# Optimization experiments

Hardware: AMD Instinct MI355X
Metric: run time of the kernel (lower is better)

## Reference

```python
import jax, jax.numpy as jnp
import numpy as np

N_NODES = 50000
N_EDGES = 800000
FEAT = 128
HID1 = 128
HID2 = 64


def setup_inputs() -> dict:
    key = jax.random.key(0)
    k = jax.random.split(key, 6)
    x = jax.random.normal(k[0], (N_NODES, FEAT), dtype=jnp.float32)
    edge_index = jax.random.randint(k[1], (2, N_EDGES), 0, N_NODES, dtype=jnp.int32)
    # Glorot-style init scaling like PyG's GCNConv linear
    W1 = jax.random.normal(k[2], (FEAT, HID1), dtype=jnp.float32) * (1.0 / np.sqrt(FEAT))
    b1 = jnp.zeros((HID1,), dtype=jnp.float32)
    W2 = jax.random.normal(k[3], (HID1, HID2), dtype=jnp.float32) * (1.0 / np.sqrt(HID1))
    b2 = jnp.zeros((HID2,), dtype=jnp.float32)
    return {"x": x, "edge_index": edge_index, "W1": W1, "b1": b1, "W2": W2, "b2": b2}


def _gcn_conv(x, src, dst, W, b, n_nodes):
    """PyG GCNConv: h = X W; out_i = sum_j norm_ij h_j + b, with self-loops and
    symmetric normalization norm_ij = deg_i^-1/2 * deg_j^-1/2 (deg counts self-loop)."""
    h = x @ W  # [N, out]
    # degree at target nodes (self-loops already appended to src/dst)
    deg = jax.ops.segment_sum(jnp.ones_like(dst, dtype=h.dtype), dst, num_segments=n_nodes)
    dinv = jax.lax.rsqrt(jnp.maximum(deg, 1.0))  # deg >= 1 because of self-loops
    norm = dinv[src] * dinv[dst]  # [E+N]
    msg = h[src] * norm[:, None]  # gather + scale, [E+N, out]
    out = jax.ops.segment_sum(msg, dst, num_segments=n_nodes)
    return out + b


def reference(x, edge_index, W1, b1, W2, b2):
    n = x.shape[0]
    self_idx = jnp.arange(n, dtype=edge_index.dtype)
    src = jnp.concatenate([edge_index[0], self_idx])
    dst = jnp.concatenate([edge_index[1], self_idx])
    h = jax.nn.relu(_gcn_conv(x, src, dst, W1, b1, n))
    out = _gcn_conv(h, src, dst, W2, b2, n)
    return out
```

## Files before the change

### kernel.cpp

```cpp
#include <hip/hip_runtime.h>
#include <hip/hip_bf16.h>


typedef __attribute__((ext_vector_type(8))) short short8;
typedef __attribute__((ext_vector_type(4))) float f32x4;

__device__ __forceinline__ float bf_lo(unsigned u) { return __uint_as_float(u << 16); }
__device__ __forceinline__ float bf_hi(unsigned u) { return __uint_as_float(u & 0xffff0000u); }
__device__ __forceinline__ unsigned short f2bf(float f) {
    return (unsigned short)(__bfloat16_as_ushort(__float2bfloat16(f)));
}

__global__ __launch_bounds__(256) void setup_kernel(int* __restrict__ cnt, int N,
                                                    const float* __restrict__ W1,
                                                    unsigned short* __restrict__ Wp1,
                                                    const float* __restrict__ W2,
                                                    unsigned short* __restrict__ Wp2) {
    int i = blockIdx.x * 256 + threadIdx.x;
    if (i < N + 1) {
        cnt[i] = 0;
    } else if (i < N + 1 + 128 * 128) {
        int q = i - (N + 1);
        int j = q & 7;
        int n = (q >> 3) & 127;
        int kb = q >> 10;
        Wp1[q] = f2bf(W1[(kb * 8 + j) * 128 + n]);
    } else if (i < N + 1 + 128 * 128 + 128 * 64) {
        int q = i - (N + 1) - 128 * 128;
        int j = q & 7;
        int n = (q >> 3) & 63;
        int kb = q >> 9;
        Wp2[q] = f2bf(W2[(kb * 8 + j) * 64 + n]);
    }
}

__global__ __launch_bounds__(256) void count_kernel(const int* __restrict__ dst,
                                                    int* __restrict__ cnt,
                                                    int* __restrict__ eslot, int E) {
    int e = blockIdx.x * 256 + threadIdx.x;
    if (e < E) eslot[e] = atomicAdd(&cnt[dst[e]], 1);
}

__global__ __launch_bounds__(256) void alloc_kernel(int* __restrict__ cnt,
                                                    int* __restrict__ row_ptr,
                                                    float* __restrict__ dinv, int N) {
    int i = blockIdx.x * 256 + threadIdx.x;
    int lane = threadIdx.x & 63;
    int c = (i < N) ? cnt[i] : 0;
    if (i < N) dinv[i] = rsqrtf((float)(c + 1));
    int incl = c;
#pragma unroll
    for (int off = 1; off < 64; off <<= 1) {
        int u = __shfl_up(incl, off, 64);
        if (lane >= off) incl += u;
    }
    int base = 0;
    if (lane == 63) base = atomicAdd(&cnt[N], incl);
    base = __shfl(base, 63, 64);
    if (i < N) row_ptr[i] = base + incl - c;
}

__global__ __launch_bounds__(256) void scatgemm_kernel(
    const int* __restrict__ src, const int* __restrict__ dst,
    const int* __restrict__ row_ptr, const int* __restrict__ eslot,
    int* __restrict__ ssrc, int E,
    const float* __restrict__ X, const unsigned short* __restrict__ Wp1,
    const float* __restrict__ dinv, unsigned short* __restrict__ g1,
    int N, int gb) {
    if ((int)blockIdx.x >= gb) {
        int e = (blockIdx.x - gb) * 256 + threadIdx.x;
        if (e < E) {
            int p = row_ptr[dst[e]] + eslot[e];
            ssrc[p] = src[e];
        }
        return;
    }
    constexpr int NT = 8;
    const int lane = threadIdx.x & 63;
    const int wave = threadIdx.x >> 6;
    const int col = lane & 15;
    const int quad = lane >> 4;
    const int row0w = (blockIdx.x * 4 + wave) * 16;

    int arow = row0w + col;
    if (arow >= N) arow = N - 1;

    short8 afr[4];
    const float* Xr = X + (size_t)arow * 128;
#pragma unroll
    for (int c = 0; c < 4; ++c) {
        float4 f0 = *(const float4*)(Xr + c * 32 + quad * 8);
        float4 f1 = *(const float4*)(Xr + c * 32 + quad * 8 + 4);
        short8 a;
        a[0] = (short)f2bf(f0.x); a[1] = (short)f2bf(f0.y);
        a[2] = (short)f2bf(f0.z); a[3] = (short)f2bf(f0.w);
        a[4] = (short)f2bf(f1.x); a[5] = (short)f2bf(f1.y);
        a[6] = (short)f2bf(f1.z); a[7] = (short)f2bf(f1.w);
        afr[c] = a;
    }

    f32x4 acc[NT];
#pragma unroll
    for (int t = 0; t < NT; ++t) acc[t] = (f32x4){0.f, 0.f, 0.f, 0.f};

    const uint4* Wq = (const uint4*)Wp1;
#pragma unroll
    for (int c = 0; c < 4; ++c) {
        short8 bfr[NT];
#pragma unroll
        for (int t = 0; t < NT; ++t) {
            union { uint4 u; short8 s; } cv;
            cv.u = Wq[(size_t)(c * 4 + quad) * 128 + t * 16 + col];
            bfr[t] = cv.s;
        }
#pragma unroll
        for (int t = 0; t < NT; ++t)
            acc[t] = __builtin_amdgcn_mfma_f32_16x16x32_bf16(afr[c], bfr[t], acc[t], 0, 0, 0);
    }

#pragma unroll
    for (int r = 0; r < 4; ++r) {
        int row = row0w + quad * 4 + r;
        if (row < N) {
            float dv = dinv[row];
#pragma unroll
            for (int t = 0; t < NT; ++t)
                g1[(size_t)row * 128 + t * 16 + col] = f2bf(acc[t][r] * dv);
        }
    }
}

template <int M>
__global__ __launch_bounds__(256) void mfma_gemm_kernel(const unsigned short* __restrict__ A,
                                                        const unsigned short* __restrict__ Wp,
                                                        const float* __restrict__ dinv,
                                                        unsigned short* __restrict__ C,
                                                        int N) {
    constexpr int NT = M / 16;
    const int lane = threadIdx.x & 63;
    const int wave = threadIdx.x >> 6;
    const int col = lane & 15;
    const int quad = lane >> 4;
    const int row0w = (blockIdx.x * 4 + wave) * 16;

    int arow = row0w + col;
    if (arow >= N) arow = N - 1;

    short8 afr[4];
    const uint4* Z = (const uint4*)A;
#pragma unroll
    for (int c = 0; c < 4; ++c) {
        union { uint4 u; short8 s; } cv;
        cv.u = Z[(size_t)arow * 16 + c * 4 + quad];
        afr[c] = cv.s;
    }

    f32x4 acc[NT];
#pragma unroll
    for (int t = 0; t < NT; ++t) acc[t] = (f32x4){0.f, 0.f, 0.f, 0.f};

    const uint4* Wq = (const uint4*)Wp;
#pragma unroll
    for (int c = 0; c < 4; ++c) {
        short8 bfr[NT];
#pragma unroll
        for (int t = 0; t < NT; ++t) {
            union { uint4 u; short8 s; } cv;
            cv.u = Wq[(size_t)(c * 4 + quad) * M + t * 16 + col];
            bfr[t] = cv.s;
        }
#pragma unroll
        for (int t = 0; t < NT; ++t)
            acc[t] = __builtin_amdgcn_mfma_f32_16x16x32_bf16(afr[c], bfr[t], acc[t], 0, 0, 0);
    }

#pragma unroll
    for (int r = 0; r < 4; ++r) {
        int row = row0w + quad * 4 + r;
        if (row < N) {
            float dv = dinv[row];
#pragma unroll
            for (int t = 0; t < NT; ++t)
                C[(size_t)row * M + t * 16 + col] = f2bf(acc[t][r] * dv);
        }
    }
}

template <int M, bool RELU, bool OUTBF16>
__global__ __launch_bounds__(256) void agg_kernel(const unsigned short* __restrict__ g,
                                                  const int* __restrict__ row_ptr,
                                                  const int* __restrict__ cnt,
                                                  const int* __restrict__ ssrc,
                                                  const float* __restrict__ dinv,
                                                  const float* __restrict__ bias,
                                                  void* __restrict__ outraw, int N) {
    int node = __builtin_amdgcn_readfirstlane((int)(blockIdx.x * 4 + (threadIdx.x >> 6)));
    if (node >= N) return;
    int lane = threadIdx.x & 63;
    float di = dinv[node];
    int beg = row_ptr[node];
    int end = beg + cnt[node];

    if constexpr (M == 128) {
        const unsigned* hp = (const unsigned*)g;
        unsigned hv = hp[node * 64 + lane];
        float ax0 = bf_lo(hv), ay0 = bf_hi(hv);
        float ax1 = 0.f, ay1 = 0.f;
        int j = beg;
        for (; j + 7 < end; j += 8) {
            int s0 = ssrc[j + 0], s1 = ssrc[j + 1], s2 = ssrc[j + 2], s3 = ssrc[j + 3];
            int s4 = ssrc[j + 4], s5 = ssrc[j + 5], s6 = ssrc[j + 6], s7 = ssrc[j + 7];
            unsigned v0 = hp[s0 * 64 + lane], v1 = hp[s1 * 64 + lane];
            unsigned v2 = hp[s2 * 64 + lane], v3 = hp[s3 * 64 + lane];
            unsigned v4 = hp[s4 * 64 + lane], v5 = hp[s5 * 64 + lane];
            unsigned v6 = hp[s6 * 64 + lane], v7 = hp[s7 * 64 + lane];
            ax0 += bf_lo(v0) + bf_lo(v1) + bf_lo(v2) + bf_lo(v3);
            ax1 += bf_lo(v4) + bf_lo(v5) + bf_lo(v6) + bf_lo(v7);
            ay0 += bf_hi(v0) + bf_hi(v1) + bf_hi(v2) + bf_hi(v3);
            ay1 += bf_hi(v4) + bf_hi(v5) + bf_hi(v6) + bf_hi(v7);
        }
        for (; j + 3 < end; j += 4) {
            int s0 = ssrc[j + 0], s1 = ssrc[j + 1], s2 = ssrc[j + 2], s3 = ssrc[j + 3];
            unsigned v0 = hp[s0 * 64 + lane], v1 = hp[s1 * 64 + lane];
            unsigned v2 = hp[s2 * 64 + lane], v3 = hp[s3 * 64 + lane];
            ax0 += bf_lo(v0) + bf_lo(v1);
            ax1 += bf_lo(v2) + bf_lo(v3);
            ay0 += bf_hi(v0) + bf_hi(v1);
            ay1 += bf_hi(v2) + bf_hi(v3);
        }
        for (; j < end; ++j) {
            unsigned v = hp[ssrc[j] * 64 + lane];
            ax0 += bf_lo(v);
            ay0 += bf_hi(v);
        }
        float ax = (ax0 + ax1) * di + bias[2 * lane];
        float ay = (ay0 + ay1) * di + bias[2 * lane + 1];
        if (RELU) { ax = fmaxf(ax, 0.f); ay = fmaxf(ay, 0.f); }
        if constexpr (OUTBF16) {
            unsigned pk = (unsigned)f2bf(ax) | ((unsigned)f2bf(ay) << 16);
            ((unsigned*)outraw)[node * 64 + lane] = pk;
        } else {
            ((float2*)outraw)[node * 64 + lane] = make_float2(ax, ay);
        }
    } else {
        float a0 = __uint_as_float((unsigned)g[node * 64 + lane] << 16);
        float a1 = 0.f;
        int j = beg;
        for (; j + 7 < end; j += 8) {
            int s0 = ssrc[j + 0], s1 = ssrc[j + 1], s2 = ssrc[j + 2], s3 = ssrc[j + 3];
            int s4 = ssrc[j + 4], s5 = ssrc[j + 5], s6 = ssrc[j + 6], s7 = ssrc[j + 7];
            float v0 = __uint_as_float((unsigned)g[s0 * 64 + lane] << 16);
            float v1 = __uint_as_float((unsigned)g[s1 * 64 + lane] << 16);
            float v2 = __uint_as_float((unsigned)g[s2 * 64 + lane] << 16);
            float v3 = __uint_as_float((unsigned)g[s3 * 64 + lane] << 16);
            float v4 = __uint_as_float((unsigned)g[s4 * 64 + lane] << 16);
            float v5 = __uint_as_float((unsigned)g[s5 * 64 + lane] << 16);
            float v6 = __uint_as_float((unsigned)g[s6 * 64 + lane] << 16);
            float v7 = __uint_as_float((unsigned)g[s7 * 64 + lane] << 16);
            a0 += v0 + v1 + v2 + v3;
            a1 += v4 + v5 + v6 + v7;
        }
        for (; j + 3 < end; j += 4) {
            int s0 = ssrc[j + 0], s1 = ssrc[j + 1], s2 = ssrc[j + 2], s3 = ssrc[j + 3];
            float v0 = __uint_as_float((unsigned)g[s0 * 64 + lane] << 16);
            float v1 = __uint_as_float((unsigned)g[s1 * 64 + lane] << 16);
            float v2 = __uint_as_float((unsigned)g[s2 * 64 + lane] << 16);
            float v3 = __uint_as_float((unsigned)g[s3 * 64 + lane] << 16);
            a0 += v0 + v1;
            a1 += v2 + v3;
        }
        for (; j < end; ++j)
            a0 += __uint_as_float((unsigned)g[ssrc[j] * 64 + lane] << 16);
        float acc = (a0 + a1) * di + bias[lane];
        if (RELU) acc = fmaxf(acc, 0.f);
        if constexpr (OUTBF16) {
            ((unsigned short*)outraw)[node * 64 + lane] = f2bf(acc);
        } else {
            ((float*)outraw)[node * 64 + lane] = acc;
        }
    }
}

extern "C" void kernel_launch(void* const* d_in, const int* in_sizes, int n_in,
                              void* d_out, int out_size, void* d_ws, size_t ws_size,
                              hipStream_t stream) {
    const float* x = (const float*)d_in[0];
    const int* eidx = (const int*)d_in[1];
    const float* W1 = (const float*)d_in[2];
    const float* b1 = (const float*)d_in[3];
    const float* W2 = (const float*)d_in[4];
    const float* b2 = (const float*)d_in[5];
    float* out = (float*)d_out;

    const int N = in_sizes[0] / 128;
    const int E = in_sizes[1] / 2;
    const int* src = eidx;
    const int* dst = eidx + E;

    char* ws = (char*)d_ws;
    size_t off = 0;
    auto alloc = [&](size_t bytes) -> char* {
        char* p = ws + off;
        off = (off + bytes + 255) & ~(size_t)255;
        return p;
    };
    int* cnt = (int*)alloc((size_t)(N + 1) * 4);
    int* row_ptr = (int*)alloc((size_t)N * 4);
    int* eslot = (int*)alloc((size_t)E * 4);
    int* ssrc = (int*)alloc((size_t)E * 4);
    float* dinv = (float*)alloc((size_t)N * 4);
    unsigned short* Wp1 = (unsigned short*)alloc(128 * 128 * 2);
    unsigned short* Wp2 = (unsigned short*)alloc(128 * 64 * 2);
    unsigned short* g1 = (unsigned short*)alloc((size_t)N * 128 * 2);
    unsigned short* z1 = (unsigned short*)alloc((size_t)N * 128 * 2);
    unsigned short* g2 = (unsigned short*)alloc((size_t)N * 64 * 2);

    const int nbN = (N + 255) / 256;
    const int nbE = (E + 255) / 256;
    const int gb = (N + 63) / 64;
    const int setup_n = N + 1 + 128 * 128 + 128 * 64;

    setup_kernel<<<(setup_n + 255) / 256, 256, 0, stream>>>(cnt, N, W1, Wp1, W2, Wp2);
    count_kernel<<<nbE, 256, 0, stream>>>(dst, cnt, eslot, E);
    alloc_kernel<<<nbN, 256, 0, stream>>>(cnt, row_ptr, dinv, N);
    scatgemm_kernel<<<gb + nbE, 256, 0, stream>>>(src, dst, row_ptr, eslot, ssrc, E,
                                                  x, Wp1, dinv, g1, N, gb);
    agg_kernel<128, true, true><<<(N + 3) / 4, 256, 0, stream>>>(g1, row_ptr, cnt, ssrc, dinv, b1, z1, N);
    mfma_gemm_kernel<64><<<gb, 256, 0, stream>>>(z1, Wp2, dinv, g2, N);
    agg_kernel<64, false, false><<<(N + 3) / 4, 256, 0, stream>>>(g2, row_ptr, cnt, ssrc, dinv, b2, out, N);
}
```

Baseline: 208.1 us.

## Fuse layer-1 aggregation with layer-2 GEMM via shared-memory tile

Merges the first-layer aggregation (with bias and ReLU) and the second-layer MFMA GEMM into one kernel. Each block aggregates 16 nodes into a bf16 tile in LDS, then each wave computes 16 output columns from that tile. This removes the z1 intermediate buffer and its global write and read, plus one kernel launch. In exchange, the gather phase now runs with 16 nodes per block and needs a __syncthreads before the GEMM, which could change latency hiding for the irregular gathers.

```diff
diff --git a/kernel.cpp b/kernel.cpp
--- a/kernel.cpp
+++ b/kernel.cpp
@@ -130,70 +130,106 @@
     }
 }
 
-template <int M>
-__global__ __launch_bounds__(256) void mfma_gemm_kernel(const unsigned short* __restrict__ A,
-                                                        const unsigned short* __restrict__ Wp,
-                                                        const float* __restrict__ dinv,
-                                                        unsigned short* __restrict__ C,
-                                                        int N) {
-    constexpr int NT = M / 16;
+__global__ __launch_bounds__(256) void aggmm_kernel(const unsigned short* __restrict__ g1,
+                                                    const int* __restrict__ row_ptr,
+                                                    const int* __restrict__ cnt,
+                                                    const int* __restrict__ ssrc,
+                                                    const float* __restrict__ dinv,
+                                                    const float* __restrict__ b1,
+                                                    const unsigned short* __restrict__ Wp2,
+                                                    unsigned short* __restrict__ g2, int N) {
+    __shared__ unsigned short zt[16][136];
+    __shared__ float sdinv[16];
     const int lane = threadIdx.x & 63;
     const int wave = threadIdx.x >> 6;
+    const int nodebase = blockIdx.x * 16;
+    const unsigned* hp = (const unsigned*)g1;
+
+    const float bx = b1[2 * lane];
+    const float by = b1[2 * lane + 1];
+
+#pragma unroll
+    for (int k = 0; k < 4; ++k) {
+        int zr = wave * 4 + k;
+        int node = __builtin_amdgcn_readfirstlane(nodebase + zr);
+        unsigned pk = 0;
+        if (node < N) {
+            float di = dinv[node];
+            int beg = row_ptr[node];
+            int end = beg + cnt[node];
+            unsigned hv = hp[node * 64 + lane];
+            float ax0 = bf_lo(hv), ay0 = bf_hi(hv);
+            float ax1 = 0.f, ay1 = 0.f;
+            int j = beg;
+            for (; j + 7 < end; j += 8) {
+                int s0 = ssrc[j + 0], s1 = ssrc[j + 1], s2 = ssrc[j + 2], s3 = ssrc[j + 3];
+                int s4 = ssrc[j + 4], s5 = ssrc[j + 5], s6 = ssrc[j + 6], s7 = ssrc[j + 7];
+                unsigned v0 = hp[s0 * 64 + lane], v1 = hp[s1 * 64 + lane];
+                unsigned v2 = hp[s2 * 64 + lane], v3 = hp[s3 * 64 + lane];
+                unsigned v4 = hp[s4 * 64 + lane], v5 = hp[s5 * 64 + lane];
+                unsigned v6 = hp[s6 * 64 + lane], v7 = hp[s7 * 64 + lane];
+                ax0 += bf_lo(v0) + bf_lo(v1) + bf_lo(v2) + bf_lo(v3);
+                ax1 += bf_lo(v4) + bf_lo(v5) + bf_lo(v6) + bf_lo(v7);
+                ay0 += bf_hi(v0) + bf_hi(v1) + bf_hi(v2) + bf_hi(v3);
+                ay1 += bf_hi(v4) + bf_hi(v5) + bf_hi(v6) + bf_hi(v7);
+            }
+            for (; j + 3 < end; j += 4) {
+                int s0 = ssrc[j + 0], s1 = ssrc[j + 1], s2 = ssrc[j + 2], s3 = ssrc[j + 3];
+                unsigned v0 = hp[s0 * 64 + lane], v1 = hp[s1 * 64 + lane];
+                unsigned v2 = hp[s2 * 64 + lane], v3 = hp[s3 * 64 + lane];
+                ax0 += bf_lo(v0) + bf_lo(v1);
+                ax1 += bf_lo(v2) + bf_lo(v3);
+                ay0 += bf_hi(v0) + bf_hi(v1);
+                ay1 += bf_hi(v2) + bf_hi(v3);
+            }
+            for (; j < end; ++j) {
+                unsigned v = hp[ssrc[j] * 64 + lane];
+                ax0 += bf_lo(v);
+                ay0 += bf_hi(v);
+            }
+            float ax = fmaxf((ax0 + ax1) * di + bx, 0.f);
+            float ay = fmaxf((ay0 + ay1) * di + by, 0.f);
+            pk = (unsigned)f2bf(ax) | ((unsigned)f2bf(ay) << 16);
+            if (lane == 0) sdinv[zr] = di;
+        } else if (lane == 0) {
+            sdinv[zr] = 0.f;
+        }
+        ((unsigned*)&zt[zr][0])[lane] = pk;
+    }
+    __syncthreads();
+
     const int col = lane & 15;
     const int quad = lane >> 4;
-    const int row0w = (blockIdx.x * 4 + wave) * 16;
-
-    int arow = row0w + col;
-    if (arow >= N) arow = N - 1;
-
     short8 afr[4];
-    const uint4* Z = (const uint4*)A;
 #pragma unroll
     for (int c = 0; c < 4; ++c) {
         union { uint4 u; short8 s; } cv;
-        cv.u = Z[(size_t)arow * 16 + c * 4 + quad];
+        cv.u = *(const uint4*)&zt[col][c * 32 + quad * 8];
         afr[c] = cv.s;
     }
-
-    f32x4 acc[NT];
-#pragma unroll
-    for (int t = 0; t < NT; ++t) acc[t] = (f32x4){0.f, 0.f, 0.f, 0.f};
-
-    const uint4* Wq = (const uint4*)Wp;
+    f32x4 acc = (f32x4){0.f, 0.f, 0.f, 0.f};
+    const uint4* Wq = (const uint4*)Wp2;
 #pragma unroll
     for (int c = 0; c < 4; ++c) {
-        short8 bfr[NT];
-#pragma unroll
-        for (int t = 0; t < NT; ++t) {
-            union { uint4 u; short8 s; } cv;
-            cv.u = Wq[(size_t)(c * 4 + quad) * M + t * 16 + col];
-            bfr[t] = cv.s;
-        }
-#pragma unroll
-        for (int t = 0; t < NT; ++t)
-            acc[t] = __builtin_amdgcn_mfma_f32_16x16x32_bf16(afr[c], bfr[t], acc[t], 0, 0, 0);
-    }
-
+        union { uint4 u; short8 s; } cv;
+        cv.u = Wq[(size_t)(c * 4 + quad) * 64 + wave * 16 + col];
+        acc = __builtin_amdgcn_mfma_f32_16x16x32_bf16(afr[c], cv.s, acc, 0, 0, 0);
+    }
 #pragma unroll
     for (int r = 0; r < 4; ++r) {
-        int row = row0w + quad * 4 + r;
-        if (row < N) {
-            float dv = dinv[row];
-#pragma unroll
-            for (int t = 0; t < NT; ++t)
-                C[(size_t)row * M + t * 16 + col] = f2bf(acc[t][r] * dv);
-        }
-    }
-}
-
-template <int M, bool RELU, bool OUTBF16>
-__global__ __launch_bounds__(256) void agg_kernel(const unsigned short* __restrict__ g,
-                                                  const int* __restrict__ row_ptr,
-                                                  const int* __restrict__ cnt,
-                                                  const int* __restrict__ ssrc,
-                                                  const float* __restrict__ dinv,
-                                                  const float* __restrict__ bias,
-                                                  void* __restrict__ outraw, int N) {
+        int row = nodebase + quad * 4 + r;
+        if (row < N)
+            g2[(size_t)row * 64 + wave * 16 + col] = f2bf(acc[r] * sdinv[quad * 4 + r]);
+    }
+}
+
+__global__ __launch_bounds__(256) void agg2_kernel(const unsigned short* __restrict__ g,
+                                                   const int* __restrict__ row_ptr,
+                                                   const int* __restrict__ cnt,
+                                                   const int* __restrict__ ssrc,
+                                                   const float* __restrict__ dinv,
+                                                   const float* __restrict__ bias,
+                                                   float* __restrict__ out, int N) {
     int node = __builtin_amdgcn_readfirstlane((int)(blockIdx.x * 4 + (threadIdx.x >> 6)));
     if (node >= N) return;
     int lane = threadIdx.x & 63;
@@ -201,84 +237,35 @@
     int beg = row_ptr[node];
     int end = beg + cnt[node];
 
-    if constexpr (M == 128) {
-        const unsigned* hp = (const unsigned*)g;
-        unsigned hv = hp[node * 64 + lane];
-        float ax0 = bf_lo(hv), ay0 = bf_hi(hv);
-        float ax1 = 0.f, ay1 = 0.f;
-        int j = beg;
-        for (; j + 7 < end; j += 8) {
-            int s0 = ssrc[j + 0], s1 = ssrc[j + 1], s2 = ssrc[j + 2], s3 = ssrc[j + 3];
-            int s4 = ssrc[j + 4], s5 = ssrc[j + 5], s6 = ssrc[j + 6], s7 = ssrc[j + 7];
-            unsigned v0 = hp[s0 * 64 + lane], v1 = hp[s1 * 64 + lane];
-            unsigned v2 = hp[s2 * 64 + lane], v3 = hp[s3 * 64 + lane];
-            unsigned v4 = hp[s4 * 64 + lane], v5 = hp[s5 * 64 + lane];
-            unsigned v6 = hp[s6 * 64 + lane], v7 = hp[s7 * 64 + lane];
-            ax0 += bf_lo(v0) + bf_lo(v1) + bf_lo(v2) + bf_lo(v3);
-            ax1 += bf_lo(v4) + bf_lo(v5) + bf_lo(v6) + bf_lo(v7);
-            ay0 += bf_hi(v0) + bf_hi(v1) + bf_hi(v2) + bf_hi(v3);
-            ay1 += bf_hi(v4) + bf_hi(v5) + bf_hi(v6) + bf_hi(v7);
-        }
-        for (; j + 3 < end; j += 4) {
-            int s0 = ssrc[j + 0], s1 = ssrc[j + 1], s2 = ssrc[j + 2], s3 = ssrc[j + 3];
-            unsigned v0 = hp[s0 * 64 + lane], v1 = hp[s1 * 64 + lane];
-            unsigned v2 = hp[s2 * 64 + lane], v3 = hp[s3 * 64 + lane];
-            ax0 += bf_lo(v0) + bf_lo(v1);
-            ax1 += bf_lo(v2) + bf_lo(v3);
-            ay0 += bf_hi(v0) + bf_hi(v1);
-            ay1 += bf_hi(v2) + bf_hi(v3);
-        }
-        for (; j < end; ++j) {
-            unsigned v = hp[ssrc[j] * 64 + lane];
-            ax0 += bf_lo(v);
-            ay0 += bf_hi(v);
-        }
-        float ax = (ax0 + ax1) * di + bias[2 * lane];
-        float ay = (ay0 + ay1) * di + bias[2 * lane + 1];
-        if (RELU) { ax = fmaxf(ax, 0.f); ay = fmaxf(ay, 0.f); }
-        if constexpr (OUTBF16) {
-            unsigned pk = (unsigned)f2bf(ax) | ((unsigned)f2bf(ay) << 16);
-            ((unsigned*)outraw)[node * 64 + lane] = pk;
-        } else {
-            ((float2*)outraw)[node * 64 + lane] = make_float2(ax, ay);
-        }
-    } else {
-        float a0 = __uint_as_float((unsigned)g[node * 64 + lane] << 16);
-        float a1 = 0.f;
-        int j = beg;
-        for (; j + 7 < end; j += 8) {
-            int s0 = ssrc[j + 0], s1 = ssrc[j + 1], s2 = ssrc[j + 2], s3 = ssrc[j + 3];
-            int s4 = ssrc[j + 4], s5 = ssrc[j + 5], s6 = ssrc[j + 6], s7 = ssrc[j + 7];
-            float v0 = __uint_as_float((unsigned)g[s0 * 64 + lane] << 16);
-            float v1 = __uint_as_float((unsigned)g[s1 * 64 + lane] << 16);
-            float v2 = __uint_as_float((unsigned)g[s2 * 64 + lane] << 16);
-            float v3 = __uint_as_float((unsigned)g[s3 * 64 + lane] << 16);
-            float v4 = __uint_as_float((unsigned)g[s4 * 64 + lane] << 16);
-            float v5 = __uint_as_float((unsigned)g[s5 * 64 + lane] << 16);
-            float v6 = __uint_as_float((unsigned)g[s6 * 64 + lane] << 16);
-            float v7 = __uint_as_float((unsigned)g[s7 * 64 + lane] << 16);
-            a0 += v0 + v1 + v2 + v3;
-            a1 += v4 + v5 + v6 + v7;
-        }
-        for (; j + 3 < end; j += 4) {
-            int s0 = ssrc[j + 0], s1 = ssrc[j + 1], s2 = ssrc[j + 2], s3 = ssrc[j + 3];
-            float v0 = __uint_as_float((unsigned)g[s0 * 64 + lane] << 16);
-            float v1 = __uint_as_float((unsigned)g[s1 * 64 + lane] << 16);
-            float v2 = __uint_as_float((unsigned)g[s2 * 64 + lane] << 16);
-            float v3 = __uint_as_float((unsigned)g[s3 * 64 + lane] << 16);
-            a0 += v0 + v1;
-            a1 += v2 + v3;
-        }
-        for (; j < end; ++j)
-            a0 += __uint_as_float((unsigned)g[ssrc[j] * 64 + lane] << 16);
-        float acc = (a0 + a1) * di + bias[lane];
-        if (RELU) acc = fmaxf(acc, 0.f);
-        if constexpr (OUTBF16) {
-            ((unsigned short*)outraw)[node * 64 + lane] = f2bf(acc);
-        } else {
-            ((float*)outraw)[node * 64 + lane] = acc;
-        }
-    }
+    float a0 = __uint_as_float((unsigned)g[node * 64 + lane] << 16);
+    float a1 = 0.f;
+    int j = beg;
+    for (; j + 7 < end; j += 8) {
+        int s0 = ssrc[j + 0], s1 = ssrc[j + 1], s2 = ssrc[j + 2], s3 = ssrc[j + 3];
+        int s4 = ssrc[j + 4], s5 = ssrc[j + 5], s6 = ssrc[j + 6], s7 = ssrc[j + 7];
+        float v0 = __uint_as_float((unsigned)g[s0 * 64 + lane] << 16);
+        float v1 = __uint_as_float((unsigned)g[s1 * 64 + lane] << 16);
+        float v2 = __uint_as_float((unsigned)g[s2 * 64 + lane] << 16);
+        float v3 = __uint_as_float((unsigned)g[s3 * 64 + lane] << 16);
+        float v4 = __uint_as_float((unsigned)g[s4 * 64 + lane] << 16);
+        float v5 = __uint_as_float((unsigned)g[s5 * 64 + lane] << 16);
+        float v6 = __uint_as_float((unsigned)g[s6 * 64 + lane] << 16);
+        float v7 = __uint_as_float((unsigned)g[s7 * 64 + lane] << 16);
+        a0 += v0 + v1 + v2 + v3;
+        a1 += v4 + v5 + v6 + v7;
+    }
+    for (; j + 3 < end; j += 4) {
+        int s0 = ssrc[j + 0], s1 = ssrc[j + 1], s2 = ssrc[j + 2], s3 = ssrc[j + 3];
+        float v0 = __uint_as_float((unsigned)g[s0 * 64 + lane] << 16);
+        float v1 = __uint_as_float((unsigned)g[s1 * 64 + lane] << 16);
+        float v2 = __uint_as_float((unsigned)g[s2 * 64 + lane] << 16);
+        float v3 = __uint_as_float((unsigned)g[s3 * 64 + lane] << 16);
+        a0 += v0 + v1;
+        a1 += v2 + v3;
+    }
+    for (; j < end; ++j)
+        a0 += __uint_as_float((unsigned)g[ssrc[j] * 64 + lane] << 16);
+    out[node * 64 + lane] = (a0 + a1) * di + bias[lane];
 }
 
 extern "C" void kernel_launch(void* const* d_in, const int* in_sizes, int n_in,
@@ -312,7 +299,6 @@
     unsigned short* Wp1 = (unsigned short*)alloc(128 * 128 * 2);
     unsigned short* Wp2 = (unsigned short*)alloc(128 * 64 * 2);
     unsigned short* g1 = (unsigned short*)alloc((size_t)N * 128 * 2);
-    unsigned short* z1 = (unsigned short*)alloc((size_t)N * 128 * 2);
     unsigned short* g2 = (unsigned short*)alloc((size_t)N * 64 * 2);
 
     const int nbN = (N + 255) / 256;
@@ -325,7 +311,6 @@
     alloc_kernel<<<nbN, 256, 0, stream>>>(cnt, row_ptr, dinv, N);
     scatgemm_kernel<<<gb + nbE, 256, 0, stream>>>(src, dst, row_ptr, eslot, ssrc, E,
                                                   x, Wp1, dinv, g1, N, gb);
-    agg_kernel<128, true, true><<<(N + 3) / 4, 256, 0, stream>>>(g1, row_ptr, cnt, ssrc, dinv, b1, z1, N);
-    mfma_gemm_kernel<64><<<gb, 256, 0, stream>>>(z1, Wp2, dinv, g2, N);
-    agg_kernel<64, false, false><<<(N + 3) / 4, 256, 0, stream>>>(g2, row_ptr, cnt, ssrc, dinv, b2, out, N);
-}
+    aggmm_kernel<<<(N + 15) / 16, 256, 0, stream>>>(g1, row_ptr, cnt, ssrc, dinv, b1, Wp2, g2, N);
+    agg2_kernel<<<(N + 3) / 4, 256, 0, stream>>>(g2, row_ptr, cnt, ssrc, dinv, b2, out, N);
+}
```

Measured after the change: 200.6 us. 3.6% less time.

## Split aggregation into feature slices with four edges per wave in parallel

Applied to the files above, without the earlier changes.

Replaces the one-wave-per-node aggregation kernels with sliced versions. Each block handles one 64-byte feature slice for 16 nodes, and each wave processes four edges at once across 16-lane groups, then combines the partial sums with shuffles. Adjacent blocks work on the same nodes' slices, so the gathered working set per block shrinks and L2 locality may improve. In exchange each node's index list is reread once per slice, lanes are wasted in the tail iterations, and the final stores issue from only a quarter of the lanes.

```diff
diff --git a/kernel.cpp b/kernel.cpp
--- a/kernel.cpp
+++ b/kernel.cpp
@@ -130,13 +130,68 @@
     }
 }
 
-template <int M>
+__global__ __launch_bounds__(256) void agg1s_kernel(const unsigned short* __restrict__ g1,
+                                                    const int* __restrict__ row_ptr,
+                                                    const int* __restrict__ cnt,
+                                                    const int* __restrict__ ssrc,
+                                                    const float* __restrict__ dinv,
+                                                    const float* __restrict__ b1,
+                                                    unsigned short* __restrict__ z1,
+                                                    int N) {
+    const int slice = blockIdx.x & 3;
+    const int group = blockIdx.x >> 2;
+    const int lane = threadIdx.x & 63;
+    const int wave = threadIdx.x >> 6;
+    const int e = lane >> 4;
+    const int u = lane & 15;
+    const unsigned* hp = (const unsigned*)g1;
+    const int soff = slice * 16 + u;
+
+    const float blo = b1[slice * 32 + 2 * u];
+    const float bhi = b1[slice * 32 + 2 * u + 1];
+
+#pragma unroll
+    for (int k = 0; k < 4; ++k) {
+        int node = group * 16 + wave * 4 + k;
+        if (node >= N) break;
+        float di = dinv[node];
+        int beg = row_ptr[node];
+        int c0 = cnt[node];
+        unsigned sv = hp[(size_t)node * 64 + soff];
+        float alo = 0.f, ahi = 0.f;
+        int it = 0;
+        for (; it + 8 <= c0; it += 8) {
+            int s0 = ssrc[beg + it + e];
+            int s1 = ssrc[beg + it + 4 + e];
+            unsigned v0 = hp[(size_t)s0 * 64 + soff];
+            unsigned v1 = hp[(size_t)s1 * 64 + soff];
+            alo += bf_lo(v0) + bf_lo(v1);
+            ahi += bf_hi(v0) + bf_hi(v1);
+        }
+        for (; it < c0; it += 4) {
+            int idx = it + e;
+            bool valid = idx < c0;
+            int s = valid ? ssrc[beg + idx] : node;
+            unsigned v = hp[(size_t)s * 64 + soff];
+            if (valid) { alo += bf_lo(v); ahi += bf_hi(v); }
+        }
+        alo += __shfl_xor(alo, 16, 64); alo += __shfl_xor(alo, 32, 64);
+        ahi += __shfl_xor(ahi, 16, 64); ahi += __shfl_xor(ahi, 32, 64);
+        float zlo = fmaxf((alo + bf_lo(sv)) * di + blo, 0.f);
+        float zhi = fmaxf((ahi + bf_hi(sv)) * di + bhi, 0.f);
+        if (e == 0) {
+            unsigned pk = (unsigned)f2bf(zlo) | ((unsigned)f2bf(zhi) << 16);
+            ((unsigned*)z1)[(size_t)node * 64 + soff] = pk;
+        }
+    }
+}
+
 __global__ __launch_bounds__(256) void mfma_gemm_kernel(const unsigned short* __restrict__ A,
                                                         const unsigned short* __restrict__ Wp,
                                                         const float* __restrict__ dinv,
                                                         unsigned short* __restrict__ C,
                                                         int N) {
-    constexpr int NT = M / 16;
+    constexpr int M = 64, NT = 4;
     const int lane = threadIdx.x & 63;
     const int wave = threadIdx.x >> 6;
     const int col = lane & 15;
@@ -186,97 +241,57 @@
     }
 }
 
-template <int M, bool RELU, bool OUTBF16>
-__global__ __launch_bounds__(256) void agg_kernel(const unsigned short* __restrict__ g,
-                                                  const int* __restrict__ row_ptr,
-                                                  const int* __restrict__ cnt,
-                                                  const int* __restrict__ ssrc,
-                                                  const float* __restrict__ dinv,
-                                                  const float* __restrict__ bias,
-                                                  void* __restrict__ outraw, int N) {
-    int node = __builtin_amdgcn_readfirstlane((int)(blockIdx.x * 4 + (threadIdx.x >> 6)));
-    if (node >= N) return;
-    int lane = threadIdx.x & 63;
-    float di = dinv[node];
-    int beg = row_ptr[node];
-    int end = beg + cnt[node];
-
-    if constexpr (M == 128) {
-        const unsigned* hp = (const unsigned*)g;
-        unsigned hv = hp[node * 64 + lane];
-        float ax0 = bf_lo(hv), ay0 = bf_hi(hv);
-        float ax1 = 0.f, ay1 = 0.f;
-        int j = beg;
-        for (; j + 7 < end; j += 8) {
-            int s0 = ssrc[j + 0], s1 = ssrc[j + 1], s2 = ssrc[j + 2], s3 = ssrc[j + 3];
-            int s4 = ssrc[j + 4], s5 = ssrc[j + 5], s6 = ssrc[j + 6], s7 = ssrc[j + 7];
-            unsigned v0 = hp[s0 * 64 + lane], v1 = hp[s1 * 64 + lane];
-            unsigned v2 = hp[s2 * 64 + lane], v3 = hp[s3 * 64 + lane];
-            unsigned v4 = hp[s4 * 64 + lane], v5 = hp[s5 * 64 + lane];
-            unsigned v6 = hp[s6 * 64 + lane], v7 = hp[s7 * 64 + lane];
-            ax0 += bf_lo(v0) + bf_lo(v1) + bf_lo(v2) + bf_lo(v3);
-            ax1 += bf_lo(v4) + bf_lo(v5) + bf_lo(v6) + bf_lo(v7);
-            ay0 += bf_hi(v0) + bf_hi(v1) + bf_hi(v2) + bf_hi(v3);
-            ay1 += bf_hi(v4) + bf_hi(v5) + bf_hi(v6) + bf_hi(v7);
-        }
-        for (; j + 3 < end; j += 4) {
-            int s0 = ssrc[j + 0], s1 = ssrc[j + 1], s2 = ssrc[j + 2], s3 = ssrc[j + 3];
-            unsigned v0 = hp[s0 * 64 + lane], v1 = hp[s1 * 64 + lane];
-            unsigned v2 = hp[s2 * 64 + lane], v3 = hp[s3 * 64 + lane];
-            ax0 += bf_lo(v0) + bf_lo(v1);
-            ax1 += bf_lo(v2) + bf_lo(v3);
-            ay0 += bf_hi(v0) + bf_hi(v1);
-            ay1 += bf_hi(v2) + bf_hi(v3);
-        }
-        for (; j < end; ++j) {
-            unsigned v = hp[ssrc[j] * 64 + lane];
-            ax0 += bf_lo(v);
-            ay0 += bf_hi(v);
-        }
-        float ax = (ax0 + ax1) * di + bias[2 * lane];
-        float ay = (ay0 + ay1) * di + bias[2 * lane + 1];
-        if (RELU) { ax = fmaxf(ax, 0.f); ay = fmaxf(ay, 0.f); }
-        if constexpr (OUTBF16) {
-            unsigned pk = (unsigned)f2bf(ax) | ((unsigned)f2bf(ay) << 16);
-            ((unsigned*)outraw)[node * 64 + lane] = pk;
-        } else {
-            ((float2*)outraw)[node * 64 + lane] = make_float2(ax, ay);
-        }
-    } else {
-        float a0 = __uint_as_float((unsigned)g[node * 64 + lane] << 16);
-        float a1 = 0.f;
-        int j = beg;
-        for (; j + 7 < end; j += 8) {
-            int s0 = ssrc[j + 0], s1 = ssrc[j + 1], s2 = ssrc[j + 2], s3 = ssrc[j + 3];
-            int s4 = ssrc[j + 4], s5 = ssrc[j + 5], s6 = ssrc[j + 6], s7 = ssrc[j + 7];
-            float v0 = __uint_as_float((unsigned)g[s0 * 64 + lane] << 16);
-            float v1 = __uint_as_float((unsigned)g[s1 * 64 + lane] << 16);
-            float v2 = __uint_as_float((unsigned)g[s2 * 64 + lane] << 16);
-            float v3 = __uint_as_float((unsigned)g[s3 * 64 + lane] << 16);
-            float v4 = __uint_as_float((unsigned)g[s4 * 64 + lane] << 16);
-            float v5 = __uint_as_float((unsigned)g[s5 * 64 + lane] << 16);
-            float v6 = __uint_as_float((unsigned)g[s6 * 64 + lane] << 16);
-            float v7 = __uint_as_float((unsigned)g[s7 * 64 + lane] << 16);
-            a0 += v0 + v1 + v2 + v3;
-            a1 += v4 + v5 + v6 + v7;
-        }
-        for (; j + 3 < end; j += 4) {
-            int s0 = ssrc[j + 0], s1 = ssrc[j + 1], s2 = ssrc[j + 2], s3 = ssrc[j + 3];
-            float v0 = __uint_as_float((unsigned)g[s0 * 64 + lane] << 16);
-            float v1 = __uint_as_float((unsigned)g[s1 * 64 + lane] << 16);
-            float v2 = __uint_as_float((unsigned)g[s2 * 64 + lane] << 16);
-            float v3 = __uint_as_float((unsigned)g[s3 * 64 + lane] << 16);
-            a0 += v0 + v1;
-            a1 += v2 + v3;
-        }
-        for (; j < end; ++j)
-            a0 += __uint_as_float((unsigned)g[ssrc[j] * 64 + lane] << 16);
-        float acc = (a0 + a1) * di + bias[lane];
-        if (RELU) acc = fmaxf(acc, 0.f);
-        if constexpr (OUTBF16) {
-            ((unsigned short*)outraw)[node * 64 + lane] = f2bf(acc);
-        } else {
-            ((float*)outraw)[node * 64 + lane] = acc;
+__global__ __launch_bounds__(256) void agg2s_kernel(const unsigned short* __restrict__ g2,
+                                                    const int* __restrict__ row_ptr,
+                                                    const int* __restrict__ cnt,
+                                                    const int* __restrict__ ssrc,
+                                                    const float* __restrict__ dinv,
+                                                    const float* __restrict__ b2,
+                                                    float* __restrict__ out, int N) {
+    const int slice = blockIdx.x & 1;
+    const int group = blockIdx.x >> 1;
+    const int lane = threadIdx.x & 63;
+    const int wave = threadIdx.x >> 6;
+    const int e = lane >> 4;
+    const int u = lane & 15;
+    const unsigned* hp = (const unsigned*)g2;
+    const int soff = slice * 16 + u;
+
+    const float blo = b2[slice * 32 + 2 * u];
+    const float bhi = b2[slice * 32 + 2 * u + 1];
+
+#pragma unroll
+    for (int k = 0; k < 4; ++k) {
+        int node = group * 16 + wave * 4 + k;
+        if (node >= N) break;
+        float di = dinv[node];
+        int beg = row_ptr[node];
+        int c0 = cnt[node];
+        unsigned sv = hp[(size_t)node * 32 + soff];
+        float alo = 0.f, ahi = 0.f;
+        int it = 0;
+        for (; it + 8 <= c0; it += 8) {
+            int s0 = ssrc[beg + it + e];
+            int s1 = ssrc[beg + it + 4 + e];
+            unsigned v0 = hp[(size_t)s0 * 32 + soff];
+            unsigned v1 = hp[(size_t)s1 * 32 + soff];
+            alo += bf_lo(v0) + bf_lo(v1);
+            ahi += bf_hi(v0) + bf_hi(v1);
+        }
+        for (; it < c0; it += 4) {
+            int idx = it + e;
+            bool valid = idx < c0;
+            int s = valid ? ssrc[beg + idx] : node;
+            unsigned v = hp[(size_t)s * 32 + soff];
+            if (valid) { alo += bf_lo(v); ahi += bf_hi(v); }
+        }
+        alo += __shfl_xor(alo, 16, 64); alo += __shfl_xor(alo, 32, 64);
+        ahi += __shfl_xor(ahi, 16, 64); ahi += __shfl_xor(ahi, 32, 64);
+        if (e == 0) {
+            float2 o;
+            o.x = (alo + bf_lo(sv)) * di + blo;
+            o.y = (ahi + bf_hi(sv)) * di + bhi;
+            *(float2*)(out + (size_t)node * 64 + slice * 32 + 2 * u) = o;
         }
     }
 }
@@ -318,6 +333,7 @@
     const int nbN = (N + 255) / 256;
     const int nbE = (E + 255) / 256;
     const int gb = (N + 63) / 64;
+    const int ng = (N + 15) / 16;
     const int setup_n = N + 1 + 128 * 128 + 128 * 64;
 
     setup_kernel<<<(setup_n + 255) / 256, 256, 0, stream>>>(cnt, N, W1, Wp1, W2, Wp2);
@@ -325,7 +341,7 @@
     alloc_kernel<<<nbN, 256, 0, stream>>>(cnt, row_ptr, dinv, N);
     scatgemm_kernel<<<gb + nbE, 256, 0, stream>>>(src, dst, row_ptr, eslot, ssrc, E,
                                                   x, Wp1, dinv, g1, N, gb);
-    agg_kernel<128, true, true><<<(N + 3) / 4, 256, 0, stream>>>(g1, row_ptr, cnt, ssrc, dinv, b1, z1, N);
-    mfma_gemm_kernel<64><<<gb, 256, 0, stream>>>(z1, Wp2, dinv, g2, N);
-    agg_kernel<64, false, false><<<(N + 3) / 4, 256, 0, stream>>>(g2, row_ptr, cnt, ssrc, dinv, b2, out, N);
-}
+    agg1s_kernel<<<ng * 4, 256, 0, stream>>>(g1, row_ptr, cnt, ssrc, dinv, b1, z1, N);
+    mfma_gemm_kernel<<<gb, 256, 0, stream>>>(z1, Wp2, dinv, g2, N);
+    agg2s_kernel<<<ng * 2, 256, 0, stream>>>(g2, row_ptr, cnt, ssrc, dinv, b2, out, N);
+}
```

New measurement: 265.4 us. 1.27x slower.
